# Optimization experiments

Hardware: AMD Instinct MI355X
Metric: run time of the kernel (lower is better)

## Reference

```python
import jax, jax.numpy as jnp
import numpy as np

N_VOXELS = 262144
MAX_PTS = 32
C = 4
N_PATCHES = 2048          # total patches across the batch
VOXELS_PER_PATCH = 128    # N_PATCHES * 128 == N_VOXELS
BATCH = 4
PATCH_PER_SAMPLE = 512    # BATCH * 512 == N_PATCHES


def setup_inputs() -> dict:
    key = jax.random.key(0)
    k1, k2, k3, k4 = jax.random.split(key, 4)
    patch_voxels = jax.random.normal(k1, (N_VOXELS, MAX_PTS, C), dtype=jnp.float32)
    patch_voxel_num_points = jax.random.randint(k2, (N_VOXELS,), 0, MAX_PTS + 1, dtype=jnp.int32)
    patch_voxel_coords = jax.random.randint(k3, (N_VOXELS, 4), 0, 256, dtype=jnp.int32)
    # counts per patch; must sum to N_VOXELS (constant counts for a fixed-shape reference)
    patch_voxel_num_array = jnp.ones((N_PATCHES,), dtype=jnp.int32) * VOXELS_PER_PATCH
    valid_patch_center_array = jax.random.normal(k4, (N_PATCHES, 2), dtype=jnp.float32)
    valid_patch_num_array = jnp.ones((BATCH,), dtype=jnp.int32) * PATCH_PER_SAMPLE
    return {
        'patch_voxels': patch_voxels,
        'patch_voxel_num_points': patch_voxel_num_points,
        'patch_voxel_coords': patch_voxel_coords,
        'patch_voxel_num_array': patch_voxel_num_array,
        'valid_patch_center_array': valid_patch_center_array,
        'valid_patch_num_array': valid_patch_num_array,
    }


def reference(patch_voxels, patch_voxel_num_points, patch_voxel_coords,
              patch_voxel_num_array, valid_patch_center_array, valid_patch_num_array):
    # --- voxel mean pooling: sum over points, divide by clamped point count ---
    points_sum = patch_voxels.sum(axis=1)                                  # [N, C]
    normalizer = jnp.clip(patch_voxel_num_points.astype(patch_voxels.dtype), 1.0)[:, None]
    voxel_features = points_sum / normalizer                               # [N, C]

    # --- vectorized segment-id assignment (replaces the per-patch Python loop) ---
    # voxel j belongs to patch i where cumsum[i-1] <= j < cumsum[i]
    accu = jnp.cumsum(patch_voxel_num_array)                               # [P]
    n = patch_voxels.shape[0]
    batch_ids = jnp.searchsorted(accu, jnp.arange(n, dtype=accu.dtype), side='right')
    voxel_coords = patch_voxel_coords.at[:, 0].set(batch_ids.astype(patch_voxel_coords.dtype))

    # --- patch centers padded with z = 0 (flat array instead of per-sample list) ---
    z_pad = jnp.zeros((valid_patch_center_array.shape[0], 1), dtype=jnp.float32)
    patch_center_xyz = jnp.concatenate([valid_patch_center_array, z_pad], axis=-1)  # [V, 3]

    patch_num_list = valid_patch_num_array.astype(jnp.int32)
    return voxel_features, voxel_coords, patch_center_xyz, patch_num_list
```

## Files before the change

kernel.cpp:

```cpp
#include <hip/hip_runtime.h>


#define P_MAX 4096

__global__ __launch_bounds__(256) void fused_all_kernel(
    const float4* __restrict__ pv,
    const int*    __restrict__ npts,
    const int4*   __restrict__ coords,
    const int*    __restrict__ counts,
    const float*  __restrict__ centers,
    const int*    __restrict__ nums,
    float4* __restrict__ out0,
    float4* __restrict__ out1,
    float*  __restrict__ out2,
    float*  __restrict__ out3,
    int n_voxels, int P, int V, int B,
    int meanBlocks, int ppb)
{
    __shared__ int s_accu[P_MAX];
    __shared__ int s_wsum[4];

    const int b = blockIdx.x;
    const int tid = threadIdx.x;

    if (b < meanBlocks) {
        const int voxel = b * 32 + (tid >> 3);
        const int t = tid & 7;
        if (voxel >= n_voxels) return;

        const float4* base = pv + (size_t)voxel * 32;
        float4 a0 = base[t + 0];
        float4 a1 = base[t + 8];
        float4 a2 = base[t + 16];
        float4 a3 = base[t + 24];
        int np = (t == 0) ? npts[voxel] : 0;

        float sx = a0.x + a1.x + a2.x + a3.x;
        float sy = a0.y + a1.y + a2.y + a3.y;
        float sz = a0.z + a1.z + a2.z + a3.z;
        float sw = a0.w + a1.w + a2.w + a3.w;
#pragma unroll
        for (int m = 4; m; m >>= 1) {
            sx += __shfl_xor(sx, m);
            sy += __shfl_xor(sy, m);
            sz += __shfl_xor(sz, m);
            sw += __shfl_xor(sw, m);
        }
        if (t == 0) {
            float inv = 1.0f / fmaxf((float)np, 1.0f);
            out0[voxel] = make_float4(sx * inv, sy * inv, sz * inv, sw * inv);
        }
        return;
    }

    const int cb = b - meanBlocks;

    {
        const int chunk = (P + 255) >> 8;
        const int cbeg = tid * chunk;
        const int cend = min(cbeg + chunk, P);
        int s = 0;
        for (int i = cbeg; i < cend; ++i) s += counts[i];

        const int lane = tid & 63;
        const int wave = tid >> 6;
        int acc = s;
#pragma unroll
        for (int off = 1; off < 64; off <<= 1) {
            int u = __shfl_up(acc, off);
            if (lane >= off) acc += u;
        }
        if (lane == 63) s_wsum[wave] = acc;
        __syncthreads();
        int wpre = 0;
        for (int w = 0; w < wave; ++w) wpre += s_wsum[w];
        int run = wpre + acc - s;
        for (int i = cbeg; i < cend; ++i) {
            run += counts[i];
            s_accu[i] = run;
        }
        __syncthreads();
    }

    const int pBeg = cb * ppb;
    if (pBeg < P) {
        const int pEnd = min(pBeg + ppb, P);
        const int vBeg = (pBeg == 0) ? 0 : s_accu[pBeg - 1];
        const int vEnd = s_accu[pEnd - 1];

        for (int j = vBeg + tid; j < vEnd; j += 256) {
            int p = pBeg;
            while (p < pEnd - 1 && s_accu[p] <= j) ++p;
            int4 c = coords[j];
            out1[j] = make_float4((float)p, (float)c.y, (float)c.z, (float)c.w);
        }
    }

    if (cb == 0) {
        for (int i = tid; i < V; i += 256) {
            out2[3 * i + 0] = centers[2 * i + 0];
            out2[3 * i + 1] = centers[2 * i + 1];
            out2[3 * i + 2] = 0.0f;
        }
        for (int i = tid; i < B; i += 256) out3[i] = (float)nums[i];
    }
}

extern "C" void kernel_launch(void* const* d_in, const int* in_sizes, int n_in,
                              void* d_out, int out_size, void* d_ws, size_t ws_size,
                              hipStream_t stream) {
    const float* pv      = (const float*)d_in[0];
    const int*   npts    = (const int*)d_in[1];
    const int*   coords  = (const int*)d_in[2];
    const int*   pcounts = (const int*)d_in[3];
    const float* centers = (const float*)d_in[4];
    const int*   vnums   = (const int*)d_in[5];

    const int N = in_sizes[1];
    const int P = in_sizes[3];
    const int V = in_sizes[4] / 2;
    const int B = in_sizes[5];

    float* out0 = (float*)d_out;
    float* out1 = out0 + (size_t)N * 4;
    float* out2 = out1 + (size_t)N * 4;
    float* out3 = out2 + (size_t)V * 3;

    const int meanBlocks  = (N + 31) / 32;
    const int coordBlocks = 512;
    const int ppb         = (P + coordBlocks - 1) / coordBlocks;

    fused_all_kernel<<<meanBlocks + coordBlocks, 256, 0, stream>>>(
        (const float4*)pv, npts, (const int4*)coords, pcounts, centers, vnums,
        (float4*)out0, (float4*)out1, out2, out3,
        N, P, V, B, meanBlocks, ppb);
}
```

Measured before the change: 30.46 us.

## Merge mean-pooling and coord blocks into uniform blocks with prefetched voxel loads

Replaces the split grid (one block per 32 voxels for mean pooling plus 512 separate coordinate blocks) with 2048 uniform blocks. Each block handles 128 voxels of mean pooling and one patch's coordinate rewrite. The first two voxel batches are loaded before the per-block prefix scan so their memory latency overlaps the scan and coordinate work. The aim is fewer blocks, less launch/tail imbalance, and more loads in flight per thread. In exchange, every block now redundantly computes the full prefix scan over counts, and register pressure rises.

After: 31.00 us. About the same (+1.8%).

```diff
diff --git a/kernel.cpp b/kernel.cpp
--- a/kernel.cpp
+++ b/kernel.cpp
@@ -3,7 +3,28 @@
 
 #define P_MAX 4096
 
-__global__ __launch_bounds__(256) void fused_all_kernel(
+__device__ __forceinline__ void mean_reduce_store(
+    const float4& a0, const float4& a1, const float4& a2, const float4& a3,
+    int np, int t, int voxel, float4* __restrict__ out0)
+{
+    float sx = a0.x + a1.x + a2.x + a3.x;
+    float sy = a0.y + a1.y + a2.y + a3.y;
+    float sz = a0.z + a1.z + a2.z + a3.z;
+    float sw = a0.w + a1.w + a2.w + a3.w;
+#pragma unroll
+    for (int m = 4; m; m >>= 1) {
+        sx += __shfl_xor(sx, m);
+        sy += __shfl_xor(sy, m);
+        sz += __shfl_xor(sz, m);
+        sw += __shfl_xor(sw, m);
+    }
+    if (t == 0) {
+        float inv = 1.0f / fmaxf((float)np, 1.0f);
+        out0[voxel] = make_float4(sx * inv, sy * inv, sz * inv, sw * inv);
+    }
+}
+
+__global__ __launch_bounds__(256) void fused_persistent_kernel(
     const float4* __restrict__ pv,
     const int*    __restrict__ npts,
     const int4*   __restrict__ coords,
@@ -15,45 +36,33 @@
     float*  __restrict__ out2,
     float*  __restrict__ out3,
     int n_voxels, int P, int V, int B,
-    int meanBlocks, int ppb)
+    int vpb, int ppb)
 {
     __shared__ int s_accu[P_MAX];
     __shared__ int s_wsum[4];
 
-    const int b = blockIdx.x;
+    const int b   = blockIdx.x;
     const int tid = threadIdx.x;
+    const int t   = tid & 7;
+    const int g   = tid >> 3;
 
-    if (b < meanBlocks) {
-        const int voxel = b * 32 + (tid >> 3);
-        const int t = tid & 7;
-        if (voxel >= n_voxels) return;
+    const int vbase = b * vpb;
 
-        const float4* base = pv + (size_t)voxel * 32;
-        float4 a0 = base[t + 0];
-        float4 a1 = base[t + 8];
-        float4 a2 = base[t + 16];
-        float4 a3 = base[t + 24];
-        int np = (t == 0) ? npts[voxel] : 0;
-
-        float sx = a0.x + a1.x + a2.x + a3.x;
-        float sy = a0.y + a1.y + a2.y + a3.y;
-        float sz = a0.z + a1.z + a2.z + a3.z;
-        float sw = a0.w + a1.w + a2.w + a3.w;
-#pragma unroll
-        for (int m = 4; m; m >>= 1) {
-            sx += __shfl_xor(sx, m);
-            sy += __shfl_xor(sy, m);
-            sz += __shfl_xor(sz, m);
-            sw += __shfl_xor(sw, m);
-        }
-        if (t == 0) {
-            float inv = 1.0f / fmaxf((float)np, 1.0f);
-            out0[voxel] = make_float4(sx * inv, sy * inv, sz * inv, sw * inv);
-        }
-        return;
+    int vA = vbase + g;
+    int vB = vbase + 32 + g;
+    bool okA = vA < n_voxels, okB = vB < n_voxels;
+    float4 a0, a1, a2, a3, c0, c1, c2, c3;
+    int npA = 0, npB = 0;
+    if (okA) {
+        const float4* base = pv + (size_t)vA * 32;
+        a0 = base[t]; a1 = base[t + 8]; a2 = base[t + 16]; a3 = base[t + 24];
+        if (t == 0) npA = npts[vA];
     }
-
-    const int cb = b - meanBlocks;
+    if (okB) {
+        const float4* base = pv + (size_t)vB * 32;
+        c0 = base[t]; c1 = base[t + 8]; c2 = base[t + 16]; c3 = base[t + 24];
+        if (t == 0) npB = npts[vB];
+    }
 
     {
         const int chunk = (P + 255) >> 8;
@@ -61,7 +70,6 @@
         const int cend = min(cbeg + chunk, P);
         int s = 0;
         for (int i = cbeg; i < cend; ++i) s += counts[i];
-
         const int lane = tid & 63;
         const int wave = tid >> 6;
         int acc = s;
@@ -82,21 +90,19 @@
         __syncthreads();
     }
 
-    const int pBeg = cb * ppb;
+    const int pBeg = b * ppb;
     if (pBeg < P) {
         const int pEnd = min(pBeg + ppb, P);
-        const int vBeg = (pBeg == 0) ? 0 : s_accu[pBeg - 1];
-        const int vEnd = s_accu[pEnd - 1];
-
-        for (int j = vBeg + tid; j < vEnd; j += 256) {
+        const int sBeg = (pBeg == 0) ? 0 : s_accu[pBeg - 1];
+        const int sEnd = s_accu[pEnd - 1];
+        for (int j = sBeg + tid; j < sEnd; j += 256) {
             int p = pBeg;
             while (p < pEnd - 1 && s_accu[p] <= j) ++p;
             int4 c = coords[j];
             out1[j] = make_float4((float)p, (float)c.y, (float)c.z, (float)c.w);
         }
     }
-
-    if (cb == 0) {
+    if (b == 0) {
         for (int i = tid; i < V; i += 256) {
             out2[3 * i + 0] = centers[2 * i + 0];
             out2[3 * i + 1] = centers[2 * i + 1];
@@ -104,6 +110,25 @@
         }
         for (int i = tid; i < B; i += 256) out3[i] = (float)nums[i];
     }
+
+    if (okA) mean_reduce_store(a0, a1, a2, a3, npA, t, vA, out0);
+    if (okB) mean_reduce_store(c0, c1, c2, c3, npB, t, vB, out0);
+
+    vA = vbase + 64 + g;
+    vB = vbase + 96 + g;
+    okA = vA < n_voxels; okB = vB < n_voxels;
+    if (okA) {
+        const float4* base = pv + (size_t)vA * 32;
+        a0 = base[t]; a1 = base[t + 8]; a2 = base[t + 16]; a3 = base[t + 24];
+        if (t == 0) npA = npts[vA];
+    }
+    if (okB) {
+        const float4* base = pv + (size_t)vB * 32;
+        c0 = base[t]; c1 = base[t + 8]; c2 = base[t + 16]; c3 = base[t + 24];
+        if (t == 0) npB = npts[vB];
+    }
+    if (okA) mean_reduce_store(a0, a1, a2, a3, npA, t, vA, out0);
+    if (okB) mean_reduce_store(c0, c1, c2, c3, npB, t, vB, out0);
 }
 
 extern "C" void kernel_launch(void* const* d_in, const int* in_sizes, int n_in,
@@ -126,12 +151,12 @@
     float* out2 = out1 + (size_t)N * 4;
     float* out3 = out2 + (size_t)V * 3;
 
-    const int meanBlocks  = (N + 31) / 32;
-    const int coordBlocks = 512;
-    const int ppb         = (P + coordBlocks - 1) / coordBlocks;
+    const int vpb    = 128;
+    const int blocks = (N + vpb - 1) / vpb;
+    const int ppb    = (P + blocks - 1) / blocks;
 
-    fused_all_kernel<<<meanBlocks + coordBlocks, 256, 0, stream>>>(
+    fused_persistent_kernel<<<blocks, 256, 0, stream>>>(
         (const float4*)pv, npts, (const int4*)coords, pcounts, centers, vnums,
         (float4*)out0, (float4*)out1, out2, out3,
-        N, P, V, B, meanBlocks, ppb);
+        N, P, V, B, vpb, ppb);
 }
```

## Pipeline mean-pool loads across voxel groups and overlap with coord work

Applied to the files above, without the earlier changes.

Each block now handles 128 voxels in four software-pipelined iterations. The next group's loads are prefetched while the current group is reduced. The coordinate/segment-id work runs in the first 512 blocks and overlaps with the initial prefetch, so there are no longer separate coord-only blocks. This cuts the block count and raises loads in flight per thread, at the cost of more registers and blocks that are less uniform in work.

New measurement: 26.31 us (median of 2 runs). -13.6%, faster.

```diff
diff --git a/kernel.cpp b/kernel.cpp
--- a/kernel.cpp
+++ b/kernel.cpp
@@ -3,7 +3,28 @@
 
 #define P_MAX 4096
 
-__global__ __launch_bounds__(256) void fused_all_kernel(
+__device__ __forceinline__ void reduce_store(
+    float4 a0, float4 a1, float4 a2, float4 a3,
+    int np, int t, int voxel, float4* __restrict__ out0)
+{
+    float sx = a0.x + a1.x + a2.x + a3.x;
+    float sy = a0.y + a1.y + a2.y + a3.y;
+    float sz = a0.z + a1.z + a2.z + a3.z;
+    float sw = a0.w + a1.w + a2.w + a3.w;
+#pragma unroll
+    for (int m = 4; m; m >>= 1) {
+        sx += __shfl_xor(sx, m);
+        sy += __shfl_xor(sy, m);
+        sz += __shfl_xor(sz, m);
+        sw += __shfl_xor(sw, m);
+    }
+    if (t == 0) {
+        float inv = 1.0f / fmaxf((float)np, 1.0f);
+        out0[voxel] = make_float4(sx * inv, sy * inv, sz * inv, sw * inv);
+    }
+}
+
+__global__ __launch_bounds__(256) void fused_pipe_kernel(
     const float4* __restrict__ pv,
     const int*    __restrict__ npts,
     const int4*   __restrict__ coords,
@@ -15,94 +36,93 @@
     float*  __restrict__ out2,
     float*  __restrict__ out3,
     int n_voxels, int P, int V, int B,
-    int meanBlocks, int ppb)
+    int coordBlocks, int ppb)
 {
     __shared__ int s_accu[P_MAX];
     __shared__ int s_wsum[4];
 
-    const int b = blockIdx.x;
+    const int b   = blockIdx.x;
     const int tid = threadIdx.x;
+    const int t   = tid & 7;
+    const int g   = tid >> 3;
 
-    if (b < meanBlocks) {
-        const int voxel = b * 32 + (tid >> 3);
-        const int t = tid & 7;
-        if (voxel >= n_voxels) return;
+    const int vbase = b * 128;
 
-        const float4* base = pv + (size_t)voxel * 32;
-        float4 a0 = base[t + 0];
-        float4 a1 = base[t + 8];
-        float4 a2 = base[t + 16];
-        float4 a3 = base[t + 24];
-        int np = (t == 0) ? npts[voxel] : 0;
-
-        float sx = a0.x + a1.x + a2.x + a3.x;
-        float sy = a0.y + a1.y + a2.y + a3.y;
-        float sz = a0.z + a1.z + a2.z + a3.z;
-        float sw = a0.w + a1.w + a2.w + a3.w;
-#pragma unroll
-        for (int m = 4; m; m >>= 1) {
-            sx += __shfl_xor(sx, m);
-            sy += __shfl_xor(sy, m);
-            sz += __shfl_xor(sz, m);
-            sw += __shfl_xor(sw, m);
-        }
-        if (t == 0) {
-            float inv = 1.0f / fmaxf((float)np, 1.0f);
-            out0[voxel] = make_float4(sx * inv, sy * inv, sz * inv, sw * inv);
-        }
-        return;
+    float4 a0, a1, a2, a3;
+    int npA = 0;
+    int v0i = vbase + g;
+    bool ok0 = v0i < n_voxels;
+    if (ok0) {
+        const float4* base = pv + (size_t)v0i * 32;
+        a0 = base[t]; a1 = base[t + 8]; a2 = base[t + 16]; a3 = base[t + 24];
+        npA = npts[v0i];
     }
 
-    const int cb = b - meanBlocks;
-
-    {
-        const int chunk = (P + 255) >> 8;
-        const int cbeg = tid * chunk;
-        const int cend = min(cbeg + chunk, P);
-        int s = 0;
-        for (int i = cbeg; i < cend; ++i) s += counts[i];
-
-        const int lane = tid & 63;
-        const int wave = tid >> 6;
-        int acc = s;
+    if (b < coordBlocks) {
+        {
+            const int chunk = (P + 255) >> 8;
+            const int cbeg = tid * chunk;
+            const int cend = min(cbeg + chunk, P);
+            int s = 0;
+            for (int i = cbeg; i < cend; ++i) s += counts[i];
+            const int lane = tid & 63;
+            const int wave = tid >> 6;
+            int acc = s;
 #pragma unroll
-        for (int off = 1; off < 64; off <<= 1) {
-            int u = __shfl_up(acc, off);
-            if (lane >= off) acc += u;
+            for (int off = 1; off < 64; off <<= 1) {
+                int u = __shfl_up(acc, off);
+                if (lane >= off) acc += u;
+            }
+            if (lane == 63) s_wsum[wave] = acc;
+            __syncthreads();
+            int wpre = 0;
+            for (int w = 0; w < wave; ++w) wpre += s_wsum[w];
+            int run = wpre + acc - s;
+            for (int i = cbeg; i < cend; ++i) {
+                run += counts[i];
+                s_accu[i] = run;
+            }
+            __syncthreads();
         }
-        if (lane == 63) s_wsum[wave] = acc;
-        __syncthreads();
-        int wpre = 0;
-        for (int w = 0; w < wave; ++w) wpre += s_wsum[w];
-        int run = wpre + acc - s;
-        for (int i = cbeg; i < cend; ++i) {
-            run += counts[i];
-            s_accu[i] = run;
+        const int pBeg = b * ppb;
+        if (pBeg < P) {
+            const int pEnd = min(pBeg + ppb, P);
+            const int sBeg = (pBeg == 0) ? 0 : s_accu[pBeg - 1];
+            const int sEnd = s_accu[pEnd - 1];
+            for (int j = sBeg + tid; j < sEnd; j += 256) {
+                int p = pBeg;
+                while (p < pEnd - 1 && s_accu[p] <= j) ++p;
+                int4 c = coords[j];
+                out1[j] = make_float4((float)p, (float)c.y, (float)c.z, (float)c.w);
+            }
         }
-        __syncthreads();
-    }
-
-    const int pBeg = cb * ppb;
-    if (pBeg < P) {
-        const int pEnd = min(pBeg + ppb, P);
-        const int vBeg = (pBeg == 0) ? 0 : s_accu[pBeg - 1];
-        const int vEnd = s_accu[pEnd - 1];
-
-        for (int j = vBeg + tid; j < vEnd; j += 256) {
-            int p = pBeg;
-            while (p < pEnd - 1 && s_accu[p] <= j) ++p;
-            int4 c = coords[j];
-            out1[j] = make_float4((float)p, (float)c.y, (float)c.z, (float)c.w);
+        if (b == 0) {
+            for (int i = tid; i < V; i += 256) {
+                out2[3 * i + 0] = centers[2 * i + 0];
+                out2[3 * i + 1] = centers[2 * i + 1];
+                out2[3 * i + 2] = 0.0f;
+            }
+            for (int i = tid; i < B; i += 256) out3[i] = (float)nums[i];
         }
     }
 
-    if (cb == 0) {
-        for (int i = tid; i < V; i += 256) {
-            out2[3 * i + 0] = centers[2 * i + 0];
-            out2[3 * i + 1] = centers[2 * i + 1];
-            out2[3 * i + 2] = 0.0f;
+#pragma unroll
+    for (int it = 0; it < 4; ++it) {
+        float4 b0, b1, b2, b3;
+        int npB = 0;
+        int vNext = vbase + (it + 1) * 32 + g;
+        bool okN = (it < 3) && (vNext < n_voxels);
+        if (okN) {
+            const float4* base = pv + (size_t)vNext * 32;
+            b0 = base[t]; b1 = base[t + 8]; b2 = base[t + 16]; b3 = base[t + 24];
+            npB = npts[vNext];
         }
-        for (int i = tid; i < B; i += 256) out3[i] = (float)nums[i];
+        int vCur = vbase + it * 32 + g;
+        if (vCur < n_voxels) {
+            reduce_store(a0, a1, a2, a3, npA, t, vCur, out0);
+        }
+        a0 = b0; a1 = b1; a2 = b2; a3 = b3;
+        npA = npB;
     }
 }
 
@@ -126,12 +146,12 @@
     float* out2 = out1 + (size_t)N * 4;
     float* out3 = out2 + (size_t)V * 3;
 
-    const int meanBlocks  = (N + 31) / 32;
+    const int blocks      = (N + 127) / 128;
     const int coordBlocks = 512;
     const int ppb         = (P + coordBlocks - 1) / coordBlocks;
 
-    fused_all_kernel<<<meanBlocks + coordBlocks, 256, 0, stream>>>(
+    fused_pipe_kernel<<<blocks, 256, 0, stream>>>(
         (const float4*)pv, npts, (const int4*)coords, pcounts, centers, vnums,
         (float4*)out0, (float4*)out1, out2, out3,
-        N, P, V, B, meanBlocks, ppb);
+        N, P, V, B, coordBlocks, ppb);
 }
```
